# Performance work log

Measured on AMD Instinct MI355X. Metric: run time of the kernel, lower is better.

Reference implementation:

```python
import jax, jax.numpy as jnp
import numpy as np

B, Q, HID = 2, 2048, 2048
HQ, HKV, D = 16, 4, 128
EPS = 1e-6
THETA = 1000000.0


def _rmsnorm(x, w):
    # x: [..., D]
    return x * jax.lax.rsqrt(jnp.mean(x * x, axis=-1, keepdims=True) + EPS) * w


def _rope(x, cos, sin):
    # neox-style: split halves. x: [B,Q,H,D], cos/sin: [B,Q,1,D/2]
    d2 = x.shape[-1] // 2
    x1, x2 = x[..., :d2], x[..., d2:]
    return jnp.concatenate([x1 * cos - x2 * sin, x2 * cos + x1 * sin], axis=-1)


def setup_inputs() -> dict:
    key = jax.random.key(0)
    k1, k2, k3 = jax.random.split(key, 3)
    positions = jnp.broadcast_to(jnp.arange(Q, dtype=jnp.int32), (B, Q))
    hidden_states = jax.random.normal(k1, (B, Q, HID), dtype=jnp.float32)
    k_cache = jnp.zeros((B, HKV, Q, D), dtype=jnp.float32)
    v_cache = jnp.zeros((B, HKV, Q, D), dtype=jnp.float32)
    wqkv = jax.random.normal(k2, (HQ * D + 2 * HKV * D, HID), dtype=jnp.float32) * (HID ** -0.5)
    wo = jax.random.normal(k3, (HID, HQ * D), dtype=jnp.float32) * ((HQ * D) ** -0.5)
    q_norm_w = jnp.ones((D,), dtype=jnp.float32)
    k_norm_w = jnp.ones((D,), dtype=jnp.float32)
    return {"positions": positions, "hidden_states": hidden_states, "k_cache": k_cache,
            "v_cache": v_cache, "wqkv": wqkv, "wo": wo, "q_norm_w": q_norm_w,
            "k_norm_w": k_norm_w, "seq_len": Q}


def reference(positions, hidden_states, k_cache, v_cache, wqkv, wo, q_norm_w, k_norm_w, seq_len):
    bsz, qlen, _ = hidden_states.shape
    q_size, kv_size = HQ * D, HKV * D
    scale = D ** -0.5

    qkv = hidden_states.reshape(bsz * qlen, HID) @ wqkv.T  # [B*Q, q+2kv]
    q = qkv[:, :q_size].reshape(bsz, qlen, HQ, D)
    k = qkv[:, q_size:q_size + kv_size].reshape(bsz, qlen, HKV, D)
    v = qkv[:, q_size + kv_size:].reshape(bsz, qlen, HKV, D)

    q = _rmsnorm(q, q_norm_w)
    k = _rmsnorm(k, k_norm_w)

    inv_freq = 1.0 / (THETA ** (jnp.arange(0, D, 2, dtype=jnp.float32) / D))  # [D/2]
    freqs = positions.astype(jnp.float32)[..., None] * inv_freq  # [B,Q,D/2]
    cos = jnp.cos(freqs)[:, :, None, :]
    sin = jnp.sin(freqs)[:, :, None, :]
    q = _rope(q, cos, sin)
    k = _rope(k, cos, sin)

    q = q.transpose(0, 2, 1, 3)  # [B,HQ,Q,D]
    k = k.transpose(0, 2, 1, 3)  # [B,HKV,Q,D]
    v = v.transpose(0, 2, 1, 3)

    start = seq_len - qlen
    k_cache = jax.lax.dynamic_update_slice(k_cache, k, (0, 0, start, 0))
    v_cache = jax.lax.dynamic_update_slice(v_cache, v, (0, 0, start, 0))
    k_full = k_cache[:, :, :seq_len, :]
    v_full = v_cache[:, :, :seq_len, :]

    rep = HQ // HKV
    kf = jnp.repeat(k_full, rep, axis=1)  # [B,HQ,S,D]
    vf = jnp.repeat(v_full, rep, axis=1)

    scores = jnp.einsum('bhqd,bhkd->bhqk', q, kf) * scale
    if qlen == seq_len:  # is_causal path
        causal = jnp.tril(jnp.ones((qlen, seq_len), dtype=bool))
        scores = jnp.where(causal, scores, jnp.finfo(scores.dtype).min)
    attn = jax.nn.softmax(scores, axis=-1)
    out = jnp.einsum('bhqk,bhkd->bhqd', attn, vf)  # [B,HQ,Q,D]
    out = out.transpose(0, 2, 1, 3).reshape(bsz * qlen, HQ * D)
    return (out @ wo.T).reshape(bsz, qlen, HID)
```

## Files before the change

### kernel.cpp

```cpp
#include <hip/hip_runtime.h>

#define B_    2
#define Q_    2048
#define HID_  2048
#define HQ_   16
#define HKV_  4
#define D_    128
#define NQKV  3072
#define QS_   2048
#define KVS_  512
#define QSC_  (0.08838834764831843f * 1.4426950408889634f)
#define LOG2_THETA 19.931568569324174f

typedef unsigned short u16;
typedef __attribute__((ext_vector_type(8))) short bf16x8;
typedef __attribute__((ext_vector_type(4))) float f32x4;

__device__ __forceinline__ u16 f2bf(float x) {
  union { float f; unsigned int u; } v; v.f = x;
  unsigned int r = v.u + 0x7FFFu + ((v.u >> 16) & 1u);
  return (u16)(r >> 16);
}
__device__ __forceinline__ u16 f2bf_t(float x) {
  union { float f; unsigned int u; } v; v.f = x;
  return (u16)(v.u >> 16);
}

__device__ __forceinline__ void gl2lds16(u16* lds, const u16* g) {
  __builtin_amdgcn_global_load_lds((const __attribute__((address_space(1))) void*)g,
                                   (__attribute__((address_space(3))) void*)lds,
                                   16, 0, 0);
}

#define N4_HID  2097152
#define N4_WQKV 1572864
#define N4_WO   1048576
__global__ __launch_bounds__(256) void cvt_all(const float* __restrict__ h,
                                               const float* __restrict__ wq,
                                               const float* __restrict__ wo,
                                               u16* __restrict__ oh,
                                               u16* __restrict__ owq,
                                               u16* __restrict__ owo) {
  int i = blockIdx.x * 256 + threadIdx.x;
  const float* src; u16* dst; int off;
  if (i < N4_HID)                 { src = h;  dst = oh;  off = i; }
  else if (i < N4_HID + N4_WQKV)  { src = wq; dst = owq; off = i - N4_HID; }
  else                            { src = wo; dst = owo; off = i - N4_HID - N4_WQKV; }
  float4 v = *(const float4*)(src + (size_t)off * 4);
  ushort4 o;
  o.x = f2bf(v.x); o.y = f2bf(v.y); o.z = f2bf(v.z); o.w = f2bf(v.w);
  *(ushort4*)(dst + (size_t)off * 4) = o;
}

__global__ __launch_bounds__(256) void gemm_bt(const u16* __restrict__ A,
                                               const u16* __restrict__ Bw,
                                               float* __restrict__ C,
                                               int M, int N, int K) {
  __shared__ __align__(16) u16 As[128 * 32];
  __shared__ __align__(16) u16 Bs[128 * 32];
  const int tid = threadIdx.x;
  const int wave = tid >> 6, lane = tid & 63;
  const int wm = wave & 1, wn = wave >> 1;
  const int row16 = lane & 15, quad = lane >> 4;
  const int lr = lane >> 2, lp = lane & 3;
  const int lpg = (lp + 4 - ((lr >> 1) & 3)) & 3;
  const int swq = (((quad + (row16 >> 1)) & 3)) * 8;
  const int m0 = blockIdx.x * 128, n0 = blockIdx.y * 128;
  f32x4 acc[4][4] = {};
  for (int k0 = 0; k0 < K; k0 += 32) {
    __syncthreads();
#pragma unroll
    for (int i = 0; i < 2; i++) {
      int r = wave * 16 + i * 64 + lr;
      gl2lds16(As + (size_t)(wave * 64 + i * 256) * 8,
               A + (size_t)(m0 + r) * K + k0 + lpg * 8);
      gl2lds16(Bs + (size_t)(wave * 64 + i * 256) * 8,
               Bw + (size_t)(n0 + r) * K + k0 + lpg * 8);
    }
    __syncthreads();
    bf16x8 af[4], bfr[4];
#pragma unroll
    for (int t = 0; t < 4; t++) {
      af[t]  = *(const bf16x8*)(As + (wm * 64 + t * 16 + row16) * 32 + swq);
      bfr[t] = *(const bf16x8*)(Bs + (wn * 64 + t * 16 + row16) * 32 + swq);
    }
#pragma unroll
    for (int mi = 0; mi < 4; mi++)
#pragma unroll
      for (int ni = 0; ni < 4; ni++)
        acc[mi][ni] = __builtin_amdgcn_mfma_f32_16x16x32_bf16(af[mi], bfr[ni],
                                                              acc[mi][ni], 0, 0, 0);
  }
#pragma unroll
  for (int mi = 0; mi < 4; mi++) {
    int row = m0 + wm * 64 + mi * 16 + quad * 4;
#pragma unroll
    for (int ni = 0; ni < 4; ni++) {
      int col = n0 + wn * 64 + ni * 16 + row16;
#pragma unroll
      for (int r = 0; r < 4; r++)
        C[(size_t)(row + r) * N + col] = acc[mi][ni][r];
    }
  }
}

__global__ __launch_bounds__(256) void qk_prep(const float* __restrict__ qkv,
                                               const int* __restrict__ pos,
                                               const float* __restrict__ qw,
                                               const float* __restrict__ kw,
                                               u16* __restrict__ qb,
                                               u16* __restrict__ kb) {
  const int row = blockIdx.x;
  const int b = row >> 11, q = row & (Q_ - 1);
  const int wave = threadIdx.x >> 6, lane = threadIdx.x & 63;
  const float p = (float)pos[row];
  const float inv = exp2f(-(float)lane * (LOG2_THETA / 64.f));
  float sn, cs;
  sincosf(p * inv, &sn, &cs);
#pragma unroll
  for (int j = 0; j < 5; j++) {
    const int hh = wave * 5 + j;
    const bool isq = hh < 16;
    const int col = isq ? hh * D_ : QS_ + (hh - 16) * D_;
    const float* src = qkv + (size_t)row * NQKV + col;
    float x1 = src[lane], x2 = src[lane + 64];
    float ss = x1 * x1 + x2 * x2;
#pragma unroll
    for (int m = 1; m < 64; m <<= 1) ss += __shfl_xor(ss, m);
    const float rn = rsqrtf(ss * (1.f / 128.f) + 1e-6f);
    const float* w = isq ? qw : kw;
    float xn1 = x1 * rn * w[lane], xn2 = x2 * rn * w[lane + 64];
    float y1 = xn1 * cs - xn2 * sn;
    float y2 = xn2 * cs + xn1 * sn;
    if (isq) { y1 *= QSC_; y2 *= QSC_; }
    u16* dst = isq ? (qb + (((size_t)b * HQ_ + hh) * Q_ + q) * D_)
                   : (kb + (((size_t)b * HKV_ + (hh - 16)) * Q_ + q) * D_);
    dst[lane]      = f2bf(y1);
    dst[lane + 64] = f2bf(y2);
  }
}

__global__ __launch_bounds__(256) void v_trans(const float* __restrict__ qkv,
                                               u16* __restrict__ vt) {
  __shared__ u16 sv[64][132];
  const int q0 = blockIdx.x * 64, hk = blockIdx.y, b = blockIdx.z;
  const int tid = threadIdx.x;
#pragma unroll
  for (int i = 0; i < 8; i++) {
    int c = tid + i * 256;
    int r = c >> 5, co = (c & 31) * 4;
    float4 v = *(const float4*)(qkv + (size_t)(b * Q_ + q0 + r) * NQKV +
                                QS_ + KVS_ + hk * D_ + co);
    sv[r][co + 0] = f2bf(v.x); sv[r][co + 1] = f2bf(v.y);
    sv[r][co + 2] = f2bf(v.z); sv[r][co + 3] = f2bf(v.w);
  }
  __syncthreads();
#pragma unroll
  for (int i = 0; i < 16; i++) {
    int c = tid + i * 256;
    int d = c >> 5, qq = (c & 31) * 2;
    ushort2 o; o.x = sv[qq][d]; o.y = sv[qq + 1][d];
    *(ushort2*)(vt + ((size_t)(b * HKV_ + hk) * D_ + d) * Q_ + q0 + qq) = o;
  }
}

__global__ __launch_bounds__(256) void attn_fwd(const u16* __restrict__ qb,
                                                const u16* __restrict__ kb,
                                                const u16* __restrict__ vt,
                                                u16* __restrict__ ob) {
  __shared__ __align__(16) u16 lds[8192 + 8192 + 4608];
  u16* Ks = lds;
  u16* Vs = lds + 8192;
  u16* Ps = lds + 16384;
  const int p = blockIdx.x, h = blockIdx.y, b = blockIdx.z;
  const int hk = h >> 2;
  const int tid = threadIdx.x, wave = tid >> 6, lane = tid & 63;
  const int c = lane & 15, quad = lane >> 4;
  const int lr = lane >> 2, lp = lane & 3;
  const int lpg = (lp + 4 - ((lr >> 1) & 3)) & 3;
  const int swq = (((quad + (c >> 1)) & 3)) * 8;
  const u16* qg = qb + ((size_t)b * HQ_ + h) * (size_t)Q_ * D_;
  const u16* kg = kb + ((size_t)b * HKV_ + hk) * (size_t)Q_ * D_;
  const u16* vg = vt + ((size_t)b * HKV_ + hk) * (size_t)D_ * Q_;
  u16* Pw = Ps + wave * 1152;
  u16* Bw = Ks + wave * 2176;

#pragma unroll 1
  for (int tp = 0; tp < 2; tp++) {
    const int t = tp ? (31 - p) : p;
    const int q0 = t * 64;
    const int qrow = q0 + wave * 16 + c;
    bf16x8 qf[4];
#pragma unroll
    for (int kk = 0; kk < 4; kk++)
      qf[kk] = *(const bf16x8*)(qg + (size_t)qrow * D_ + kk * 32 + quad * 8);
    f32x4 Oa[8] = {};
    float m_run = -1e30f, l_run = 0.f;

#pragma unroll 1
    for (int kt = 0; kt <= t; kt++) {
      __syncthreads();
#pragma unroll
      for (int i = 0; i < 4; i++) {
        gl2lds16(Ks + (size_t)(i * 256 + wave * 64) * 8,
                 kg + ((size_t)kt * 64 + wave * 16 + lr) * D_ + i * 32 + lpg * 8);
        int d = (i & 1) * 64 + wave * 16 + lr;
        gl2lds16(Vs + (size_t)(i * 256 + wave * 64) * 8,
                 vg + (size_t)d * Q_ + kt * 64 + (i >> 1) * 32 + lpg * 8);
      }
      __syncthreads();
      f32x4 S[4];
#pragma unroll
      for (int n = 0; n < 4; n++) {
        f32x4 a = {};
#pragma unroll
        for (int kk = 0; kk < 4; kk++) {
          bf16x8 kf = *(const bf16x8*)(Ks + kk * 2048 + (n * 16 + c) * 32 + swq);
          a = __builtin_amdgcn_mfma_f32_16x16x32_bf16(kf, qf[kk], a, 0, 0, 0);
        }
        S[n] = a;
      }
      if (kt == t) {
#pragma unroll
        for (int n = 0; n < 4; n++)
#pragma unroll
          for (int r = 0; r < 4; r++) {
            int key = kt * 64 + n * 16 + quad * 4 + r;
            if (key > qrow) S[n][r] = -1e30f;
          }
      }
      float mx = -1e30f;
#pragma unroll
      for (int n = 0; n < 4; n++)
#pragma unroll
        for (int r = 0; r < 4; r++) mx = fmaxf(mx, S[n][r]);
      mx = fmaxf(mx, __shfl_xor(mx, 16));
      mx = fmaxf(mx, __shfl_xor(mx, 32));
      const float mn = fmaxf(m_run, mx);
      const float alpha = __builtin_amdgcn_exp2f(m_run - mn);
      m_run = mn;
      float sum = 0.f;
#pragma unroll
      for (int n = 0; n < 4; n++)
#pragma unroll
        for (int r = 0; r < 4; r++) {
          float pp = __builtin_amdgcn_exp2f(S[n][r] - mn);
          S[n][r] = pp;
          sum += pp;
        }
      sum += __shfl_xor(sum, 16);
      sum += __shfl_xor(sum, 32);
      l_run = l_run * alpha + sum;
#pragma unroll
      for (int md = 0; md < 8; md++)
#pragma unroll
        for (int r = 0; r < 4; r++) Oa[md][r] *= alpha;
#pragma unroll
      for (int n = 0; n < 4; n++) {
        short4 pk;
        pk.x = (short)f2bf_t(S[n][0]); pk.y = (short)f2bf_t(S[n][1]);
        pk.z = (short)f2bf_t(S[n][2]); pk.w = (short)f2bf_t(S[n][3]);
        *(short4*)(Pw + c * 72 + n * 16 + quad * 4) = pk;
      }
      bf16x8 pf[2];
#pragma unroll
      for (int kk2 = 0; kk2 < 2; kk2++)
        pf[kk2] = *(const bf16x8*)(Pw + c * 72 + kk2 * 32 + quad * 8);
#pragma unroll
      for (int md = 0; md < 8; md++)
#pragma unroll
        for (int kk2 = 0; kk2 < 2; kk2++) {
          bf16x8 vf = *(const bf16x8*)(Vs + kk2 * 4096 + (md * 16 + c) * 32 + swq);
          Oa[md] = __builtin_amdgcn_mfma_f32_16x16x32_bf16(vf, pf[kk2], Oa[md], 0, 0, 0);
        }
    }
    __syncthreads();
    const float invl = 1.f / l_run;
#pragma unroll
    for (int md = 0; md < 8; md++) {
      short4 ok;
      ok.x = (short)f2bf(Oa[md][0] * invl); ok.y = (short)f2bf(Oa[md][1] * invl);
      ok.z = (short)f2bf(Oa[md][2] * invl); ok.w = (short)f2bf(Oa[md][3] * invl);
      *(short4*)(Bw + c * 136 + md * 16 + quad * 4) = ok;
    }
    const int orow = q0 + wave * 16 + lr;
#pragma unroll
    for (int tt = 0; tt < 4; tt++) {
      bf16x8 ov = *(const bf16x8*)(Bw + lr * 136 + lp * 32 + tt * 8);
      *(bf16x8*)(ob + ((size_t)(b * Q_ + orow) * HQ_ + h) * D_ + lp * 32 + tt * 8) = ov;
    }
  }
}

extern "C" void kernel_launch(void* const* d_in, const int* in_sizes, int n_in,
                              void* d_out, int out_size, void* d_ws, size_t ws_size,
                              hipStream_t stream) {
  const int*   positions = (const int*)  d_in[0];
  const float* hidden    = (const float*)d_in[1];
  const float* wqkv      = (const float*)d_in[4];
  const float* wo        = (const float*)d_in[5];
  const float* qnw       = (const float*)d_in[6];
  const float* knw       = (const float*)d_in[7];
  char* ws = (char*)d_ws;
  u16*  hid_bf  = (u16*)(ws);
  u16*  wqkv_bf = (u16*)(ws + 16777216);
  u16*  wo_bf   = (u16*)(ws + 29360128);
  float* qkv    = (float*)(ws + 37748736);
  u16*  q_bf    = (u16*)(ws + 88080384);
  u16*  k_bf    = (u16*)(ws + 104857600);
  u16*  vt_bf   = (u16*)(ws + 109051904);
  u16*  attn_bf = hid_bf;

  cvt_all<<<18432, 256, 0, stream>>>(hidden, wqkv, wo, hid_bf, wqkv_bf, wo_bf);
  gemm_bt<<<dim3(32, 24), 256, 0, stream>>>(hid_bf, wqkv_bf, qkv, 4096, 3072, 2048);
  qk_prep<<<4096, 256, 0, stream>>>(qkv, positions, qnw, knw, q_bf, k_bf);
  v_trans<<<dim3(32, 4, 2), 256, 0, stream>>>(qkv, vt_bf);
  attn_fwd<<<dim3(16, 16, 2), 256, 0, stream>>>(q_bf, k_bf, vt_bf, attn_bf);
  gemm_bt<<<dim3(32, 16), 256, 0, stream>>>(attn_bf, wo_bf, (float*)d_out, 4096, 2048, 2048);
}
```

Measured before the change: 346.4 us.

## Fuse QK RMSNorm, RoPE and V transpose into QKV GEMM epilogue

The QKV projection GEMM now runs its epilogue per 128-column head tile. It applies RMSNorm, RoPE and the Q scale for Q/K heads and writes bf16 into the attention layouts, and it transposes V tiles through LDS into the V^T buffer. This removes the fp32 QKV intermediate and the separate qk_prep and v_trans kernels, saving a large round trip to global memory. A small rope_tab kernel precomputes the cos/sin table, and the GEMM's wave layout changes to 2x8 fragments per wave so each wave holds whole head rows for the norm reduction. The price is a heavier epilogue with extra LDS syncs.

After: 343.6 us. No clear change (-0.8%).

```diff
diff --git a/kernel.cpp b/kernel.cpp
--- a/kernel.cpp
+++ b/kernel.cpp
@@ -6,9 +6,6 @@
 #define HQ_   16
 #define HKV_  4
 #define D_    128
-#define NQKV  3072
-#define QS_   2048
-#define KVS_  512
 #define QSC_  (0.08838834764831843f * 1.4426950408889634f)
 #define LOG2_THETA 19.931568569324174f
 
@@ -52,6 +49,149 @@
   *(ushort4*)(dst + (size_t)off * 4) = o;
 }
 
+__global__ __launch_bounds__(256) void rope_tab(const int* __restrict__ pos,
+                                                float* __restrict__ rope) {
+  int i = blockIdx.x * 256 + threadIdx.x;
+  int d = i & 63, row = i >> 6;
+  float p = (float)pos[row];
+  float inv = exp2f(-(float)d * (LOG2_THETA / 64.f));
+  float sn, cn;
+  sincosf(p * inv, &sn, &cn);
+  float2* o = (float2*)rope;
+  o[i] = make_float2(cn, sn);
+}
+
+__global__ __launch_bounds__(256) void gemm_qkv(const u16* __restrict__ A,
+                                                const u16* __restrict__ Bw,
+                                                const float* __restrict__ rope,
+                                                const float* __restrict__ qw,
+                                                const float* __restrict__ kw,
+                                                u16* __restrict__ qb,
+                                                u16* __restrict__ kb,
+                                                u16* __restrict__ vt) {
+  __shared__ __align__(16) u16 lds[12288];
+  u16* As = lds;
+  u16* Bs = lds + 4096;
+  const int tid = threadIdx.x;
+  const int wv = tid >> 6, lane = tid & 63;
+  const int c = lane & 15, quad = lane >> 4;
+  const int lr = lane >> 2, lp = lane & 3;
+  const int lpg = (lp + 4 - ((lr >> 1) & 3)) & 3;
+  const int swq = ((quad + (c >> 1)) & 3) * 8;
+  const int m0 = blockIdx.x * 128;
+  const int by = blockIdx.y;
+  const int n0 = by * 128;
+  f32x4 acc[2][8] = {};
+  for (int k0 = 0; k0 < HID_; k0 += 32) {
+    __syncthreads();
+#pragma unroll
+    for (int i = 0; i < 2; i++) {
+      int r = wv * 16 + i * 64 + lr;
+      gl2lds16(As + (size_t)(wv * 64 + i * 256) * 8,
+               A + (size_t)(m0 + r) * HID_ + k0 + lpg * 8);
+      gl2lds16(Bs + (size_t)(wv * 64 + i * 256) * 8,
+               Bw + (size_t)(n0 + r) * HID_ + k0 + lpg * 8);
+    }
+    __syncthreads();
+    bf16x8 af[2], bfr[8];
+#pragma unroll
+    for (int mi = 0; mi < 2; mi++)
+      af[mi] = *(const bf16x8*)(As + (wv * 32 + mi * 16 + c) * 32 + swq);
+#pragma unroll
+    for (int ni = 0; ni < 8; ni++)
+      bfr[ni] = *(const bf16x8*)(Bs + (ni * 16 + c) * 32 + swq);
+#pragma unroll
+    for (int mi = 0; mi < 2; mi++)
+#pragma unroll
+      for (int ni = 0; ni < 8; ni++)
+        acc[mi][ni] = __builtin_amdgcn_mfma_f32_16x16x32_bf16(af[mi], bfr[ni],
+                                                              acc[mi][ni], 0, 0, 0);
+  }
+  __syncthreads();
+
+  if (by < 20) {
+    const bool isq = by < 16;
+    const float* w = isq ? qw : kw;
+    const float osc = isq ? QSC_ : 1.f;
+    float wl[8];
+#pragma unroll
+    for (int ni = 0; ni < 8; ni++) wl[ni] = w[ni * 16 + c];
+    u16 ob[2][4][8];
+#pragma unroll
+    for (int mi = 0; mi < 2; mi++)
+#pragma unroll
+      for (int r = 0; r < 4; r++) {
+        const int row = m0 + wv * 32 + mi * 16 + quad * 4 + r;
+        const int q = row & (Q_ - 1), b = row >> 11;
+        float ss = 0.f;
+#pragma unroll
+        for (int ni = 0; ni < 8; ni++) ss += acc[mi][ni][r] * acc[mi][ni][r];
+        ss += __shfl_xor(ss, 1); ss += __shfl_xor(ss, 2);
+        ss += __shfl_xor(ss, 4); ss += __shfl_xor(ss, 8);
+        const float rn = rsqrtf(ss * (1.f / 128.f) + 1e-6f) * osc;
+#pragma unroll
+        for (int ni = 0; ni < 4; ni++) {
+          float2 cssn = *(const float2*)(rope +
+              ((size_t)(b * Q_ + q) * 64 + ni * 16 + c) * 2);
+          float x1 = acc[mi][ni][r]     * wl[ni]     * rn;
+          float x2 = acc[mi][ni + 4][r] * wl[ni + 4] * rn;
+          ob[mi][r][ni]     = f2bf(x1 * cssn.x - x2 * cssn.y);
+          ob[mi][r][ni + 4] = f2bf(x2 * cssn.x + x1 * cssn.y);
+        }
+      }
+    u16* dstbuf = isq ? qb : kb;
+    const int hbase = isq ? (HQ_ * 0 + by) : (by - 16);
+    const int nheads = isq ? HQ_ : HKV_;
+#pragma unroll
+    for (int ph = 0; ph < 2; ph++) {
+      if (ph) __syncthreads();
+      if ((wv >> 1) == ph) {
+#pragma unroll
+        for (int mi = 0; mi < 2; mi++)
+#pragma unroll
+          for (int r = 0; r < 4; r++)
+#pragma unroll
+            for (int ni = 0; ni < 8; ni++)
+              lds[((wv & 1) * 32 + mi * 16 + quad * 4 + r) * 132 + ni * 16 + c] =
+                  ob[mi][r][ni];
+      }
+      __syncthreads();
+      const int rowg = m0 + ph * 64 + (tid >> 2);
+      const int q = rowg & (Q_ - 1), b = rowg >> 11;
+      u16* dst = dstbuf + (((size_t)(b * nheads) + hbase) * Q_ + q) * D_ + (tid & 3) * 32;
+      const u16* srcl = lds + (tid >> 2) * 132 + (tid & 3) * 32;
+#pragma unroll
+      for (int j = 0; j < 4; j++)
+        *(bf16x8*)(dst + j * 8) = *(const bf16x8*)(srcl + j * 8);
+    }
+  } else {
+    const int hk = by - 20;
+    const int bb = m0 >> 11, q0 = m0 & (Q_ - 1);
+    u16* vw = lds + wv * 3072;
+#pragma unroll
+    for (int mi = 0; mi < 2; mi++) {
+      if (mi) __syncthreads();
+#pragma unroll
+      for (int ni = 0; ni < 8; ni++) {
+        short4 pv;
+        pv.x = (short)f2bf(acc[mi][ni][0]); pv.y = (short)f2bf(acc[mi][ni][1]);
+        pv.z = (short)f2bf(acc[mi][ni][2]); pv.w = (short)f2bf(acc[mi][ni][3]);
+        *(short4*)(vw + (ni * 16 + c) * 24 + quad * 4) = pv;
+      }
+      __syncthreads();
+#pragma unroll
+      for (int it = 0; it < 2; it++) {
+        const int d = it * 64 + lane;
+        const u16* src = vw + d * 24;
+        u16* dst = vt + (((size_t)(bb * HKV_) + hk) * D_ + d) * Q_ +
+                   q0 + wv * 32 + mi * 16;
+        *(bf16x8*)(dst)     = *(const bf16x8*)(src);
+        *(bf16x8*)(dst + 8) = *(const bf16x8*)(src + 8);
+      }
+    }
+  }
+}
+
 __global__ __launch_bounds__(256) void gemm_bt(const u16* __restrict__ A,
                                                const u16* __restrict__ Bw,
                                                float* __restrict__ C,
@@ -64,7 +204,7 @@
   const int row16 = lane & 15, quad = lane >> 4;
   const int lr = lane >> 2, lp = lane & 3;
   const int lpg = (lp + 4 - ((lr >> 1) & 3)) & 3;
-  const int swq = (((quad + (row16 >> 1)) & 3)) * 8;
+  const int swq = ((quad + (row16 >> 1)) & 3) * 8;
   const int m0 = blockIdx.x * 128, n0 = blockIdx.y * 128;
   f32x4 acc[4][4] = {};
   for (int k0 = 0; k0 < K; k0 += 32) {
@@ -101,66 +241,6 @@
       for (int r = 0; r < 4; r++)
         C[(size_t)(row + r) * N + col] = acc[mi][ni][r];
     }
-  }
-}
-
-__global__ __launch_bounds__(256) void qk_prep(const float* __restrict__ qkv,
-                                               const int* __restrict__ pos,
-                                               const float* __restrict__ qw,
-                                               const float* __restrict__ kw,
-                                               u16* __restrict__ qb,
-                                               u16* __restrict__ kb) {
-  const int row = blockIdx.x;
-  const int b = row >> 11, q = row & (Q_ - 1);
-  const int wave = threadIdx.x >> 6, lane = threadIdx.x & 63;
-  const float p = (float)pos[row];
-  const float inv = exp2f(-(float)lane * (LOG2_THETA / 64.f));
-  float sn, cs;
-  sincosf(p * inv, &sn, &cs);
-#pragma unroll
-  for (int j = 0; j < 5; j++) {
-    const int hh = wave * 5 + j;
-    const bool isq = hh < 16;
-    const int col = isq ? hh * D_ : QS_ + (hh - 16) * D_;
-    const float* src = qkv + (size_t)row * NQKV + col;
-    float x1 = src[lane], x2 = src[lane + 64];
-    float ss = x1 * x1 + x2 * x2;
-#pragma unroll
-    for (int m = 1; m < 64; m <<= 1) ss += __shfl_xor(ss, m);
-    const float rn = rsqrtf(ss * (1.f / 128.f) + 1e-6f);
-    const float* w = isq ? qw : kw;
-    float xn1 = x1 * rn * w[lane], xn2 = x2 * rn * w[lane + 64];
-    float y1 = xn1 * cs - xn2 * sn;
-    float y2 = xn2 * cs + xn1 * sn;
-    if (isq) { y1 *= QSC_; y2 *= QSC_; }
-    u16* dst = isq ? (qb + (((size_t)b * HQ_ + hh) * Q_ + q) * D_)
-                   : (kb + (((size_t)b * HKV_ + (hh - 16)) * Q_ + q) * D_);
-    dst[lane]      = f2bf(y1);
-    dst[lane + 64] = f2bf(y2);
-  }
-}
-
-__global__ __launch_bounds__(256) void v_trans(const float* __restrict__ qkv,
-                                               u16* __restrict__ vt) {
-  __shared__ u16 sv[64][132];
-  const int q0 = blockIdx.x * 64, hk = blockIdx.y, b = blockIdx.z;
-  const int tid = threadIdx.x;
-#pragma unroll
-  for (int i = 0; i < 8; i++) {
-    int c = tid + i * 256;
-    int r = c >> 5, co = (c & 31) * 4;
-    float4 v = *(const float4*)(qkv + (size_t)(b * Q_ + q0 + r) * NQKV +
-                                QS_ + KVS_ + hk * D_ + co);
-    sv[r][co + 0] = f2bf(v.x); sv[r][co + 1] = f2bf(v.y);
-    sv[r][co + 2] = f2bf(v.z); sv[r][co + 3] = f2bf(v.w);
-  }
-  __syncthreads();
-#pragma unroll
-  for (int i = 0; i < 16; i++) {
-    int c = tid + i * 256;
-    int d = c >> 5, qq = (c & 31) * 2;
-    ushort2 o; o.x = sv[qq][d]; o.y = sv[qq + 1][d];
-    *(ushort2*)(vt + ((size_t)(b * HKV_ + hk) * D_ + d) * Q_ + q0 + qq) = o;
   }
 }
 
@@ -178,7 +258,7 @@
   const int c = lane & 15, quad = lane >> 4;
   const int lr = lane >> 2, lp = lane & 3;
   const int lpg = (lp + 4 - ((lr >> 1) & 3)) & 3;
-  const int swq = (((quad + (c >> 1)) & 3)) * 8;
+  const int swq = ((quad + (c >> 1)) & 3) * 8;
   const u16* qg = qb + ((size_t)b * HQ_ + h) * (size_t)Q_ * D_;
   const u16* kg = kb + ((size_t)b * HKV_ + hk) * (size_t)Q_ * D_;
   const u16* vg = vt + ((size_t)b * HKV_ + hk) * (size_t)D_ * Q_;
@@ -302,19 +382,19 @@
   const float* qnw       = (const float*)d_in[6];
   const float* knw       = (const float*)d_in[7];
   char* ws = (char*)d_ws;
-  u16*  hid_bf  = (u16*)(ws);
-  u16*  wqkv_bf = (u16*)(ws + 16777216);
-  u16*  wo_bf   = (u16*)(ws + 29360128);
-  float* qkv    = (float*)(ws + 37748736);
-  u16*  q_bf    = (u16*)(ws + 88080384);
-  u16*  k_bf    = (u16*)(ws + 104857600);
-  u16*  vt_bf   = (u16*)(ws + 109051904);
-  u16*  attn_bf = hid_bf;
+  u16*   hid_bf  = (u16*)(ws);
+  u16*   wqkv_bf = (u16*)(ws + 16777216);
+  u16*   wo_bf   = (u16*)(ws + 29360128);
+  u16*   q_bf    = (u16*)(ws + 37748736);
+  u16*   k_bf    = (u16*)(ws + 54525952);
+  u16*   vt_bf   = (u16*)(ws + 58720256);
+  float* rope    = (float*)(ws + 62914560);
+  u16*   attn_bf = hid_bf;
 
   cvt_all<<<18432, 256, 0, stream>>>(hidden, wqkv, wo, hid_bf, wqkv_bf, wo_bf);
-  gemm_bt<<<dim3(32, 24), 256, 0, stream>>>(hid_bf, wqkv_bf, qkv, 4096, 3072, 2048);
-  qk_prep<<<4096, 256, 0, stream>>>(qkv, positions, qnw, knw, q_bf, k_bf);
-  v_trans<<<dim3(32, 4, 2), 256, 0, stream>>>(qkv, vt_bf);
+  rope_tab<<<1024, 256, 0, stream>>>(positions, rope);
+  gemm_qkv<<<dim3(32, 24), 256, 0, stream>>>(hid_bf, wqkv_bf, rope, qnw, knw,
+                                             q_bf, k_bf, vt_bf);
   attn_fwd<<<dim3(16, 16, 2), 256, 0, stream>>>(q_bf, k_bf, vt_bf, attn_bf);
   gemm_bt<<<dim3(32, 16), 256, 0, stream>>>(attn_bf, wo_bf, (float*)d_out, 4096, 2048, 2048);
 }
```
